# Kernel optimization log

Measured on AMD Instinct MI355X. Metric: run time of the kernel, lower is better.

## Reference

```python
import jax, jax.numpy as jnp
import numpy as np

B, T, F, D = 2, 1, 2112, 1024
H, DH = 8, 64
INNER = H * DH
NL = 721           # cls_dim(1) + num_latents(720)
VD = 64            # vis_dim // 4
DEPTH = 6
MAX_FRAMES = 2160
EPS = 1e-5
W_SCALE = 0.02


def _ln(x, g, b):
    m = jnp.mean(x, axis=-1, keepdims=True)
    v = jnp.mean(jnp.square(x - m), axis=-1, keepdims=True)
    return (x - m) * jax.lax.rsqrt(v + EPS) * g + b


def setup_inputs() -> dict:
    key = jax.random.key(0)
    ks = jax.random.split(key, 12)
    n = lambda k, shape, s=1.0: jax.random.normal(k, shape, dtype=jnp.float32) * s
    inp = {}
    inp['x'] = n(ks[0], (B, T, F, D))
    inp['split_sizes'] = jax.random.randint(ks[1], (B,), 0, F, dtype=jnp.int32)
    # resampler parameters (randn init like torch)
    inp['latents'] = n(ks[2], (NL, D))
    inp['spatial_embs'] = n(ks[3], (VD + 1, D))
    inp['frame_embs'] = n(ks[4], (MAX_FRAMES, D))
    # per-layer attention params (stacked over depth)
    inp['nm_g'] = jnp.ones((DEPTH, D)); inp['nm_b'] = jnp.zeros((DEPTH, D))
    inp['nl_g'] = jnp.ones((DEPTH, D)); inp['nl_b'] = jnp.zeros((DEPTH, D))
    inp['wq'] = n(ks[5], (DEPTH, D, INNER), W_SCALE)
    inp['wkv'] = n(ks[6], (DEPTH, D, 2 * INNER), W_SCALE)
    inp['wo'] = n(ks[7], (DEPTH, INNER, D), W_SCALE)
    # per-layer FFN params
    inp['ffn_g'] = jnp.ones((DEPTH, D)); inp['ffn_b'] = jnp.zeros((DEPTH, D))
    inp['ffw1'] = n(ks[8], (DEPTH, D, 4 * D), W_SCALE)
    inp['ffw2'] = n(ks[9], (DEPTH, 4 * D, D), W_SCALE)
    # final norm
    inp['final_g'] = jnp.ones((D,)); inp['final_b'] = jnp.zeros((D,))
    return inp


def reference(x, split_sizes, latents, spatial_embs, frame_embs,
              nm_g, nm_b, nl_g, nl_b, wq, wkv, wo,
              ffn_g, ffn_b, ffw1, ffw2, final_g, final_b):
    b, t, f, d = x.shape
    # spatial embeddings: first VD tokens get rows [:VD], rest get row [VD] broadcast
    add_sp = jnp.concatenate(
        [spatial_embs[:VD], jnp.broadcast_to(spatial_embs[VD:VD + 1], (f - VD, d))], axis=0)
    # frame embeddings: first VD tokens get row 0, frames get rows 1..f-VD
    add_fr = jnp.concatenate(
        [jnp.broadcast_to(frame_embs[0:1], (VD, d)), frame_embs[1:f - VD + 1]], axis=0)
    x = x + (add_sp + add_fr)  # broadcast over (b, t)

    lat = jnp.broadcast_to(latents, (b, t, NL, d))

    # variable-length mask over the x part of KV; latent positions never masked
    mask_x = jnp.arange(f)[None, :] >= split_sizes[:, None]              # (b, f)
    mask = jnp.concatenate([mask_x, jnp.zeros((b, NL), dtype=bool)], -1)  # (b, f+NL)
    mask = mask[:, None, None, None, :]                                   # (b,1,1,1,j)
    scale = DH ** -0.5

    for l in range(DEPTH):
        # --- PerceiverAttention ---
        xn = _ln(x, nm_g[l], nm_b[l])
        latn = _ln(lat, nl_g[l], nl_b[l])
        q = (latn @ wq[l]).reshape(b, t, NL, H, DH) * scale
        kv = jnp.concatenate([xn, latn], axis=-2) @ wkv[l]               # (b,t,f+NL,2*inner)
        k, v = jnp.split(kv, 2, axis=-1)
        k = k.reshape(b, t, f + NL, H, DH)
        v = v.reshape(b, t, f + NL, H, DH)
        sim = jnp.einsum('btihd,btjhd->bhtij', q, k)                     # (b,h,t,NL,f+NL)
        sim = sim - jax.lax.stop_gradient(jnp.max(sim, axis=-1, keepdims=True))
        sim = jnp.where(mask, -jnp.inf, sim)
        attn = jax.nn.softmax(sim, axis=-1)
        o = jnp.einsum('bhtij,btjhd->btihd', attn, v).reshape(b, t, NL, INNER)
        lat = lat + o @ wo[l]
        # --- FeedForward ---
        h1 = _ln(lat, ffn_g[l], ffn_b[l]) @ ffw1[l]
        lat = lat + jax.nn.gelu(h1, approximate=False) @ ffw2[l]

    return _ln(lat, final_g, final_b)
```

## Files before the change

kernel.cpp:

```cpp
#include <hip/hip_runtime.h>
#include <math.h>

constexpr int B = 2;
constexpr int F = 2112;
constexpr int D = 1024;
constexpr int H = 8;
constexpr int DH = 64;
constexpr int INNER = H * DH;
constexpr int NL = 721;
constexpr int NL_PAD = 768;
constexpr int MLAT = B * NL;
constexpr int MLAT_PAD = 1536;
constexpr int VD = 64;
constexpr int DEPTH = 6;
constexpr int FN = F + NL;
constexpr int FN_PAD = 2880;
constexpr int NBH = B * H;
constexpr int SKVMAX = 8;
constexpr int MX = B * F;
constexpr float EPS = 1e-5f;

typedef __bf16 bf16x8 __attribute__((ext_vector_type(8)));
typedef float  f32x4  __attribute__((ext_vector_type(4)));

static __device__ __forceinline__ unsigned short f2bf(float f)
{
    union { float f; unsigned int u; } x; x.f = f;
    unsigned int r = x.u + 0x7FFFu + ((x.u >> 16) & 1u);
    return (unsigned short)(r >> 16);
}
static __device__ __forceinline__ float bf2f(unsigned short u)
{
    union { unsigned int i; float f; } x; x.i = ((unsigned int)u) << 16; return x.f;
}

__device__ __forceinline__ void block_reduce_2(float& s, float& ss, float* red)
{
#pragma unroll
    for (int off = 32; off; off >>= 1) {
        s  += __shfl_xor(s, off);
        ss += __shfl_xor(ss, off);
    }
    int wv = threadIdx.x >> 6;
    if ((threadIdx.x & 63) == 0) { red[wv] = s; red[4 + wv] = ss; }
    __syncthreads();
    s  = red[0] + red[1] + red[2] + red[3];
    ss = red[4] + red[5] + red[6] + red[7];
}

__global__ __launch_bounds__(256) void emb_ln_kernel(
    const float* __restrict__ x, const float* __restrict__ sp_emb,
    const float* __restrict__ fr_emb, unsigned short* __restrict__ xhat)
{
    __shared__ float red[8];
    int r = blockIdx.x;
    int j = r % F;
    int t = threadIdx.x;
    const float4* xr = (const float4*)(x + (long)r * D);
    int spr = (j < VD) ? j : VD;
    int frr = (j < VD) ? 0 : (j - VD + 1);
    const float4* sp4 = (const float4*)(sp_emb + (long)spr * D);
    const float4* fr4 = (const float4*)(fr_emb + (long)frr * D);
    float4 v = xr[t], a = sp4[t], c = fr4[t];
    v.x += a.x + c.x; v.y += a.y + c.y; v.z += a.z + c.z; v.w += a.w + c.w;
    float s  = v.x + v.y + v.z + v.w;
    float ss = v.x*v.x + v.y*v.y + v.z*v.z + v.w*v.w;
    block_reduce_2(s, ss, red);
    float mean = s * (1.0f / D);
    float var  = ss * (1.0f / D) - mean * mean;
    float rstd = rsqrtf(var + EPS);
    ushort4 o;
    o.x = f2bf((v.x - mean) * rstd);
    o.y = f2bf((v.y - mean) * rstd);
    o.z = f2bf((v.z - mean) * rstd);
    o.w = f2bf((v.w - mean) * rstd);
    ((ushort4*)(xhat + (long)r * D))[t] = o;
}

__global__ __launch_bounds__(256) void prep_a_kernel(
    const unsigned short* __restrict__ xhat, const float* __restrict__ lat,
    const float* __restrict__ nmg, const float* __restrict__ nmb,
    const float* __restrict__ nlg, const float* __restrict__ nlb,
    unsigned short* __restrict__ xa, unsigned short* __restrict__ la)
{
    __shared__ float red[8];
    int r = blockIdx.x;
    int t = threadIdx.x;
    if (r < MX) {
        ushort4 u4 = ((const ushort4*)(xhat + (long)r * D))[t];
        float4 g4 = ((const float4*)nmg)[t];
        float4 b4 = ((const float4*)nmb)[t];
        ushort4 o;
        o.x = f2bf(bf2f(u4.x) * g4.x + b4.x);
        o.y = f2bf(bf2f(u4.y) * g4.y + b4.y);
        o.z = f2bf(bf2f(u4.z) * g4.z + b4.z);
        o.w = f2bf(bf2f(u4.w) * g4.w + b4.w);
        ((ushort4*)(xa + (long)r * D))[t] = o;
    } else {
        int rr = r - MX;
        float4 v = ((const float4*)(lat + (long)rr * D))[t];
        float s  = v.x + v.y + v.z + v.w;
        float ss = v.x*v.x + v.y*v.y + v.z*v.z + v.w*v.w;
        block_reduce_2(s, ss, red);
        float mean = s * (1.0f / D);
        float var  = ss * (1.0f / D) - mean * mean;
        float rstd = rsqrtf(var + EPS);
        float4 g4 = ((const float4*)nlg)[t];
        float4 b4 = ((const float4*)nlb)[t];
        ushort4 o;
        o.x = f2bf((v.x - mean) * rstd * g4.x + b4.x);
        o.y = f2bf((v.y - mean) * rstd * g4.y + b4.y);
        o.z = f2bf((v.z - mean) * rstd * g4.z + b4.z);
        o.w = f2bf((v.w - mean) * rstd * g4.w + b4.w);
        ((ushort4*)(la + (long)rr * D))[t] = o;
    }
}

__global__ __launch_bounds__(256) void rownorm_affine_bf16_kernel(
    const float* __restrict__ in, const float* __restrict__ g,
    const float* __restrict__ b, unsigned short* __restrict__ out)
{
    __shared__ float red[8];
    int r = blockIdx.x;
    int t = threadIdx.x;
    float4 v = ((const float4*)(in + (long)r * D))[t];
    float s  = v.x + v.y + v.z + v.w;
    float ss = v.x*v.x + v.y*v.y + v.z*v.z + v.w*v.w;
    block_reduce_2(s, ss, red);
    float mean = s * (1.0f / D);
    float var  = ss * (1.0f / D) - mean * mean;
    float rstd = rsqrtf(var + EPS);
    float4 g4 = ((const float4*)g)[t];
    float4 b4 = ((const float4*)b)[t];
    ushort4 o;
    o.x = f2bf((v.x - mean) * rstd * g4.x + b4.x);
    o.y = f2bf((v.y - mean) * rstd * g4.y + b4.y);
    o.z = f2bf((v.z - mean) * rstd * g4.z + b4.z);
    o.w = f2bf((v.w - mean) * rstd * g4.w + b4.w);
    ((ushort4*)(out + (long)r * D))[t] = o;
}

__global__ __launch_bounds__(256) void final_ln_kernel(
    const float* __restrict__ in, const float* __restrict__ g,
    const float* __restrict__ b, float* __restrict__ out)
{
    __shared__ float red[8];
    int r = blockIdx.x;
    int t = threadIdx.x;
    float4 v = ((const float4*)(in + (long)r * D))[t];
    float s  = v.x + v.y + v.z + v.w;
    float ss = v.x*v.x + v.y*v.y + v.z*v.z + v.w*v.w;
    block_reduce_2(s, ss, red);
    float mean = s * (1.0f / D);
    float var  = ss * (1.0f / D) - mean * mean;
    float rstd = rsqrtf(var + EPS);
    float4 g4 = ((const float4*)g)[t];
    float4 b4 = ((const float4*)b)[t];
    float4 o;
    o.x = (v.x - mean) * rstd * g4.x + b4.x;
    o.y = (v.y - mean) * rstd * g4.y + b4.y;
    o.z = (v.z - mean) * rstd * g4.z + b4.z;
    o.w = (v.w - mean) * rstd * g4.w + b4.w;
    ((float4*)(out + (long)r * D))[t] = o;
}

__global__ __launch_bounds__(256) void lat_init_kernel(
    const float* __restrict__ latents, float* __restrict__ lat)
{
    int r = blockIdx.x;
    int i = r % NL;
    int t = threadIdx.x;
    ((float4*)(lat + (long)r * D))[t] = ((const float4*)(latents + (long)i * D))[t];
}

constexpr long WL_LAT = 1536L * 1024;
constexpr long WL_WO  = 1024L * 512;
constexpr long WL_F1  = 4096L * 1024;
constexpr long WL_F2  = 1024L * 4096;
constexpr long WL_SZ  = WL_LAT + WL_WO + WL_F1 + WL_F2;

__device__ __forceinline__ void conv_tile64(
    const float* __restrict__ src, unsigned short* __restrict__ dst,
    int Kd, int Nd, int tn, int tk, float* lds)
{
    int t = threadIdx.x;
    int n0 = tn * 64, k0 = tk * 64;
#pragma unroll
    for (int p = 0; p < 16; ++p) {
        int idx = p * 256 + t;
        int kr = idx >> 6, nc = idx & 63;
        lds[nc * 65 + kr] = src[(long)(k0 + kr) * Nd + n0 + nc];
    }
    __syncthreads();
#pragma unroll
    for (int p = 0; p < 2; ++p) {
        int nl_ = p * 32 + (t >> 3);
        int kc  = t & 7;
        unsigned short u[8];
#pragma unroll
        for (int j = 0; j < 8; ++j)
            u[j] = f2bf(lds[nl_ * 65 + kc * 8 + j]);
        *(uint4*)(dst + (long)(n0 + nl_) * Kd + k0 + kc * 8) = *(uint4*)u;
    }
}

__global__ __launch_bounds__(256) void wt_conv_all_kernel(
    const float* __restrict__ wq, const float* __restrict__ wkv,
    const float* __restrict__ wo, const float* __restrict__ ffw1,
    const float* __restrict__ ffw2,
    unsigned short* __restrict__ wbuf, long wstride, int layer0)
{
    __shared__ float lds[64 * 65];
    int l = layer0 + blockIdx.y;
    unsigned short* wl = wbuf + (long)blockIdx.y * wstride;
    const float* wq_l   = wq   + (long)l * D * INNER;
    const float* wkv_l  = wkv  + (long)l * D * 2 * INNER;
    const float* wo_l   = wo   + (long)l * INNER * D;
    const float* ffw1_l = ffw1 + (long)l * D * 4 * D;
    const float* ffw2_l = ffw2 + (long)l * 4 * D * D;

    int T = blockIdx.x;
    if (T < 128) {
        conv_tile64(wq_l, wl, D, INNER, T & 7, T >> 3, lds);
    } else if (T < 384) {
        int Ti = T - 128;
        conv_tile64(wkv_l, wl + 512L * D, D, 2 * INNER, Ti & 15, Ti >> 4, lds);
    } else if (T < 512) {
        int Ti = T - 384;
        conv_tile64(wo_l, wl + WL_LAT, INNER, D, Ti & 15, Ti >> 4, lds);
    } else if (T < 1536) {
        int Ti = T - 512;
        conv_tile64(ffw1_l, wl + WL_LAT + WL_WO, D, 4 * D, Ti & 63, Ti >> 6, lds);
    } else {
        int Ti = T - 1536;
        conv_tile64(ffw2_l, wl + WL_LAT + WL_WO + WL_F1, 4 * D, D, Ti & 15, Ti >> 4, lds);
    }
}

__device__ __forceinline__ void load_set(
    const unsigned short* __restrict__ ap, const unsigned short* __restrict__ bp,
    long rs, int ko, bf16x8 (&av)[4], bf16x8 (&bv)[4])
{
#pragma unroll
    for (int q = 0; q < 4; ++q) {
        av[q] = *(const bf16x8*)(ap + q * rs + ko);
        bv[q] = *(const bf16x8*)(bp + q * rs + ko);
    }
}

__device__ __forceinline__ void mfma_set(
    const bf16x8 (&av)[4], const bf16x8 (&bv)[4], f32x4 (&acc)[4][4])
{
#pragma unroll
    for (int mm = 0; mm < 4; ++mm)
#pragma unroll
        for (int nn = 0; nn < 4; ++nn)
            acc[mm][nn] = __builtin_amdgcn_mfma_f32_16x16x32_bf16(av[mm], bv[nn], acc[mm][nn], 0, 0, 0);
}

__device__ __forceinline__ void gemm_core(
    const unsigned short* __restrict__ ap, const unsigned short* __restrict__ bp,
    long rs, int Kc, f32x4 (&acc)[4][4])
{
    bf16x8 aC[4], bC[4], aN[4], bN[4];
    load_set(ap, bp, rs, 0, aC, bC);
    for (int ko = 0; ko < Kc; ko += 64) {
        load_set(ap, bp, rs, ko + 32, aN, bN);
        mfma_set(aC, bC, acc);
        if (ko + 64 < Kc)
            load_set(ap, bp, rs, ko + 64, aC, bC);
        mfma_set(aN, bN, acc);
    }
}

__global__ __launch_bounds__(64) void qkv_fused_kernel(
    const unsigned short* __restrict__ la, const unsigned short* __restrict__ xa,
    const unsigned short* __restrict__ wlatT,
    unsigned short* __restrict__ qb, unsigned short* __restrict__ kb,
    unsigned short* __restrict__ vt)
{
    int lane = threadIdx.x;
    int lr = lane & 15, lg = lane >> 4;

    const unsigned short* A;
    const unsigned short* Bt;
    long m0, n0;
    int M, rpb, joff, qcols;
    int T = blockIdx.x;
    if (T < 552) {
        int bm = T % 23, bn = T / 23;
        A = la; Bt = wlatT;
        m0 = (long)bm * 64; n0 = (long)bn * 64;
        M = MLAT; rpb = NL; joff = F; qcols = 512;
    } else {
        int Ti = T - 552;
        int bm = Ti % 66, bn = Ti / 66;
        A = xa; Bt = wlatT + 512L * D;
        m0 = (long)bm * 64; n0 = (long)bn * 64;
        M = MX; rpb = F; joff = 0; qcols = 0;
    }

    const unsigned short* ap = A  + (m0 + lr) * D + lg * 8;
    const unsigned short* bp = Bt + (n0 + lr) * D + lg * 8;
    f32x4 acc[4][4] = {};
    gemm_core(ap, bp, 16L * D, D, acc);

#pragma unroll
    for (int mm = 0; mm < 4; ++mm) {
        long ar0 = m0 + mm * 16 + lg * 4;
        if (ar0 >= M) continue;
#pragma unroll
        for (int nn = 0; nn < 4; ++nn) {
            long col = n0 + nn * 16 + lr;
            f32x4 v = acc[mm][nn];
            if (col < qcols) {
#pragma unroll
                for (int r = 0; r < 4; ++r) {
                    long ar = ar0 + r;
                    if (ar < M) {
                        int bb = ar >= NL;
                        long i = ar - (bb ? NL : 0);
                        qb[((long)bb * NL_PAD + i) * INNER + col] = f2bf(v[r] * 0.125f);
                    }
                }
            } else {
                int c = (int)col - qcols;
                if (c < 512) {
#pragma unroll
                    for (int r = 0; r < 4; ++r) {
                        long ar = ar0 + r;
                        if (ar < M) {
                            int bb = ar >= rpb;
                            long i = ar - (bb ? rpb : 0);
                            kb[((long)bb * FN_PAD + joff + i) * INNER + c] = f2bf(v[r]);
                        }
                    }
                } else {
                    int d = c - 512;
                    int bb0 = ar0 >= rpb;
                    int bb3 = (ar0 + 3) >= rpb;
                    long i0 = ar0 - (bb0 ? rpb : 0);
                    long j0 = joff + i0;
                    if ((ar0 + 3 < M) && (bb0 == bb3) && ((j0 & 3) == 0)) {
                        ushort4 pk;
                        pk.x = f2bf(v[0]); pk.y = f2bf(v[1]);
                        pk.z = f2bf(v[2]); pk.w = f2bf(v[3]);
                        *(ushort4*)(vt + ((long)bb0 * INNER + d) * FN_PAD + j0) = pk;
                    } else {
#pragma unroll
                        for (int r = 0; r < 4; ++r) {
                            long ar = ar0 + r;
                            if (ar < M) {
                                int bb = ar >= rpb;
                                long i = ar - (bb ? rpb : 0);
                                vt[((long)bb * INNER + d) * FN_PAD + joff + i] = f2bf(v[r]);
                            }
                        }
                    }
                }
            }
        }
    }
}

#define MODE_RESA  0
#define MODE_GELU  1

__global__ __launch_bounds__(64) void gemm_split_kernel(
    const unsigned short* __restrict__ A, const unsigned short* __restrict__ Bt,
    void* __restrict__ C, int M, int K, int Kc, int mode, int ldc)
{
    int lane = threadIdx.x;
    int lr = lane & 15, lg = lane >> 4;
    long m0 = (long)blockIdx.x * 64;
    long n0 = (long)blockIdx.y * 64;
    int k0 = blockIdx.z * Kc;

    const unsigned short* ap = A  + (m0 + lr) * K + k0 + lg * 8;
    const unsigned short* bp = Bt + (n0 + lr) * K + k0 + lg * 8;
    f32x4 acc[4][4] = {};
    gemm_core(ap, bp, 16L * K, Kc, acc);

#pragma unroll
    for (int mm = 0; mm < 4; ++mm) {
        long ar0 = m0 + mm * 16 + lg * 4;
        if (ar0 >= M) continue;
#pragma unroll
        for (int nn = 0; nn < 4; ++nn) {
            long col = n0 + nn * 16 + lr;
            f32x4 v = acc[mm][nn];
            if (mode == MODE_RESA) {
                float* p = (float*)C;
#pragma unroll
                for (int r = 0; r < 4; ++r)
                    if (ar0 + r < M)
                        unsafeAtomicAdd(&p[(ar0 + r) * (long)ldc + col], v[r]);
            } else {
                unsigned short* p = (unsigned short*)C;
#pragma unroll
                for (int r = 0; r < 4; ++r)
                    if (ar0 + r < M) {
                        float val = v[r];
                        val = 0.5f * val * (1.0f + erff(val * 0.70710678118654752f));
                        p[(ar0 + r) * (long)ldc + col] = f2bf(val);
                    }
            }
        }
    }
}

__global__ __launch_bounds__(256) void attn_split_kernel(
    const unsigned short* __restrict__ qb, const unsigned short* __restrict__ kb,
    const unsigned short* __restrict__ vt, const int* __restrict__ split,
    float* __restrict__ po, float* __restrict__ pml, int skv)
{
    int bh = blockIdx.y;
    int b  = bh >> 3;
    int h  = bh & 7;
    int sidx = blockIdx.z;
    int w  = threadIdx.x >> 6;
    int lane = threadIdx.x & 63;
    int q0 = blockIdx.x * 64 + w * 16;
    if (q0 >= NL) return;

    __shared__ unsigned short p_lds[4][16 * 64];
    unsigned short* pl = p_lds[w];

    int lr = lane & 15;
    int lg = lane >> 4;

    bf16x8 qa0, qa1;
    {
        const unsigned short* qrow = qb + ((long)b * NL_PAD + q0 + lr) * INNER + h * 64;
        qa0 = *(const bf16x8*)(qrow + lg * 8);
        qa1 = *(const bf16x8*)(qrow + 32 + lg * 8);
    }

    f32x4 oacc[4] = {{0,0,0,0},{0,0,0,0},{0,0,0,0},{0,0,0,0}};
    float m[4]    = {-1e30f, -1e30f, -1e30f, -1e30f};
    float lsum[4] = {0.f, 0.f, 0.f, 0.f};

    int sp = split[b];
    if (sp < 0) sp = 0;
    if (sp > F) sp = F;
    int ntx = (sp + 63) >> 6;
    int ntot = ntx + 12;
    int t0 = (ntot * sidx) / skv;
    int t1 = (ntot * (sidx + 1)) / skv;

    for (int t = t0; t < t1; ++t) {
        int j0, limit;
        if (t < ntx) { j0 = t * 64;             limit = sp; }
        else         { j0 = F + (t - ntx) * 64; limit = FN; }

        f32x4 s[4] = {{0,0,0,0},{0,0,0,0},{0,0,0,0},{0,0,0,0}};
        const unsigned short* kbase =
            kb + ((long)b * FN_PAD + j0 + lr) * INNER + h * 64 + lg * 8;
#pragma unroll
        for (int st = 0; st < 4; ++st) {
            bf16x8 kf0 = *(const bf16x8*)(kbase + (long)st * 16 * INNER);
            bf16x8 kf1 = *(const bf16x8*)(kbase + (long)st * 16 * INNER + 32);
            s[st] = __builtin_amdgcn_mfma_f32_16x16x32_bf16(qa0, kf0, s[st], 0, 0, 0);
            s[st] = __builtin_amdgcn_mfma_f32_16x16x32_bf16(qa1, kf1, s[st], 0, 0, 0);
        }

        if (j0 + 64 > limit) {
#pragma unroll
            for (int st = 0; st < 4; ++st) {
                bool valid = (j0 + st * 16 + lr) < limit;
#pragma unroll
                for (int r = 0; r < 4; ++r)
                    s[st][r] = valid ? s[st][r] : -1e30f;
            }
        }

        float tm[4];
#pragma unroll
        for (int r = 0; r < 4; ++r)
            tm[r] = fmaxf(fmaxf(s[0][r], s[1][r]), fmaxf(s[2][r], s[3][r]));
#pragma unroll
        for (int off = 1; off < 16; off <<= 1) {
#pragma unroll
            for (int r = 0; r < 4; ++r)
                tm[r] = fmaxf(tm[r], __shfl_xor(tm[r], off));
        }
        float cr[4];
#pragma unroll
        for (int r = 0; r < 4; ++r) {
            float mn = fmaxf(m[r], tm[r]);
            cr[r] = __expf(m[r] - mn);
            m[r]  = mn;
        }
#pragma unroll
        for (int st = 0; st < 4; ++st)
#pragma unroll
            for (int r = 0; r < 4; ++r)
                s[st][r] = __expf(s[st][r] - m[r]);
        float ts[4];
#pragma unroll
        for (int r = 0; r < 4; ++r)
            ts[r] = (s[0][r] + s[1][r]) + (s[2][r] + s[3][r]);
#pragma unroll
        for (int off = 1; off < 16; off <<= 1) {
#pragma unroll
            for (int r = 0; r < 4; ++r)
                ts[r] += __shfl_xor(ts[r], off);
        }
#pragma unroll
        for (int r = 0; r < 4; ++r)
            lsum[r] = lsum[r] * cr[r] + ts[r];
#pragma unroll
        for (int nst = 0; nst < 4; ++nst)
#pragma unroll
            for (int r = 0; r < 4; ++r)
                oacc[nst][r] *= cr[r];

#pragma unroll
        for (int st = 0; st < 4; ++st)
#pragma unroll
            for (int r = 0; r < 4; ++r) {
                int row  = lg * 4 + r;
                int col  = st * 16 + lr;
                int byte = (row * 128 + col * 2) ^ ((row & 7) << 4);
                *(unsigned short*)((char*)pl + byte) = f2bf(s[st][r]);
            }

#pragma unroll
        for (int kk = 0; kk < 2; ++kk) {
            int row  = lr;
            int byte = (row * 128 + kk * 64 + lg * 16) ^ ((row & 7) << 4);
            bf16x8 pa = *(const bf16x8*)((char*)pl + byte);
#pragma unroll
            for (int nst = 0; nst < 4; ++nst) {
                const unsigned short* vp =
                    vt + ((long)bh * DH + nst * 16 + lr) * FN_PAD + j0 + kk * 32 + lg * 8;
                bf16x8 vf = *(const bf16x8*)vp;
                oacc[nst] = __builtin_amdgcn_mfma_f32_16x16x32_bf16(pa, vf, oacc[nst], 0, 0, 0);
            }
        }
    }

    long base = ((long)sidx * NBH + bh) * NL_PAD;
#pragma unroll
    for (int nst = 0; nst < 4; ++nst)
#pragma unroll
        for (int r = 0; r < 4; ++r) {
            int row = q0 + lg * 4 + r;
            if (row < NL)
                po[(base + row) * DH + nst * 16 + lr] = oacc[nst][r];
        }
    if (lr == 0) {
#pragma unroll
        for (int r = 0; r < 4; ++r) {
            int row = q0 + lg * 4 + r;
            if (row < NL) {
                pml[(base + row) * 2 + 0] = m[r];
                pml[(base + row) * 2 + 1] = lsum[r];
            }
        }
    }
}

__global__ __launch_bounds__(256) void attn_combine_kernel(
    const float* __restrict__ po, const float* __restrict__ pml,
    unsigned short* __restrict__ o, int skv)
{
    int row = blockIdx.x * 4 + (threadIdx.x >> 6);
    if (row >= NBH * NL) return;
    int lane = threadIdx.x & 63;
    int bh = row / NL;
    int i  = row - bh * NL;
    int b = bh >> 3, h = bh & 7;

    float m = -1e30f, l = 0.0f, acc = 0.0f;
    for (int s = 0; s < skv; ++s) {
        long base = ((long)s * NBH + bh) * NL_PAD + i;
        float ms = pml[base * 2 + 0];
        float ls = pml[base * 2 + 1];
        float os = po[base * DH + lane];
        float mn = fmaxf(m, ms);
        float c1 = __expf(m - mn);
        float c2 = __expf(ms - mn);
        acc = acc * c1 + os * c2;
        l   = l * c1 + ls * c2;
        m   = mn;
    }
    o[((long)b * NL + i) * INNER + h * 64 + lane] = f2bf(acc / l);
}

extern "C" void kernel_launch(void* const* d_in, const int* in_sizes, int n_in,
                              void* d_out, int out_size, void* d_ws, size_t ws_size,
                              hipStream_t stream)
{
    const float* x        = (const float*)d_in[0];
    const int*   split    = (const int*)d_in[1];
    const float* latents  = (const float*)d_in[2];
    const float* sp_emb   = (const float*)d_in[3];
    const float* fr_emb   = (const float*)d_in[4];
    const float* nm_g     = (const float*)d_in[5];
    const float* nm_b     = (const float*)d_in[6];
    const float* nl_g     = (const float*)d_in[7];
    const float* nl_b     = (const float*)d_in[8];
    const float* wq       = (const float*)d_in[9];
    const float* wkv      = (const float*)d_in[10];
    const float* wo       = (const float*)d_in[11];
    const float* ffw1     = (const float*)d_in[12 + 2];
    const float* ffn_g    = (const float*)d_in[12];
    const float* ffn_b    = (const float*)d_in[13];
    const float* ffw2     = (const float*)d_in[15];
    const float* final_g  = (const float*)d_in[16];
    const float* final_b  = (const float*)d_in[17];
    float* out = (float*)d_out;

    char* cur = (char*)d_ws;
    auto alloc = [&](size_t bytes) {
        void* p = (void*)cur;
        cur += (bytes + 255) & ~(size_t)255;
        return p;
    };

    unsigned short* xhat = (unsigned short*)alloc((long)MX * D * 2);
    float* lat  = (float*)alloc((long)B * NL * D * 4);
    unsigned short* la  = (unsigned short*)alloc((long)MLAT_PAD * D * 2);
    unsigned short* fa  = (unsigned short*)alloc((long)MLAT_PAD * D * 2);
    unsigned short* h1b = (unsigned short*)alloc((long)MLAT_PAD * 4 * D * 2);
    unsigned short* ob  = (unsigned short*)alloc((long)MLAT_PAD * INNER * 2);
    unsigned short* qb  = (unsigned short*)alloc((long)B * NL_PAD * INNER * 2);
    unsigned short* kb  = (unsigned short*)alloc((long)B * FN_PAD * INNER * 2);
    unsigned short* vt  = (unsigned short*)alloc((long)B * FN_PAD * INNER * 2);
    unsigned short* xa  = (unsigned short*)alloc((long)MX * D * 2);
    float* pml = (float*)alloc((long)SKVMAX * NBH * NL_PAD * 2 * 4);

    size_t fixed = (size_t)(cur - (char*)d_ws);
    const size_t po8 = ((size_t)8 * NBH * NL_PAD * DH * 4 + 255) & ~(size_t)255;
    const size_t po4 = ((size_t)4 * NBH * NL_PAD * DH * 4 + 255) & ~(size_t)255;
    const size_t wb6 = ((size_t)6 * WL_SZ * 2 + 255) & ~(size_t)255;
    const size_t wb1 = ((size_t)WL_SZ * 2 + 255) & ~(size_t)255;
    const size_t margin = 4096;

    int skv;
    bool hoist_w;
    if (fixed + po8 + wb6 + margin <= ws_size)      { skv = 8; hoist_w = true;  }
    else if (fixed + po4 + wb6 + margin <= ws_size) { skv = 4; hoist_w = true;  }
    else if (fixed + po8 + wb1 + margin <= ws_size) { skv = 8; hoist_w = false; }
    else                                            { skv = 4; hoist_w = false; }

    float* po = (float*)alloc(skv == 8 ? po8 : po4);
    unsigned short* wbuf = (unsigned short*)alloc(hoist_w ? wb6 : wb1);

    emb_ln_kernel<<<MX, 256, 0, stream>>>(x, sp_emb, fr_emb, xhat);
    lat_init_kernel<<<B * NL, 256, 0, stream>>>(latents, lat);

    if (hoist_w)
        wt_conv_all_kernel<<<dim3(2560, 6), 256, 0, stream>>>(
            wq, wkv, wo, ffw1, ffw2, wbuf, WL_SZ, 0);

    for (int l = 0; l < DEPTH; ++l) {
        unsigned short* wl = wbuf + (hoist_w ? (long)l * WL_SZ : 0);
        if (!hoist_w)
            wt_conv_all_kernel<<<dim3(2560, 1), 256, 0, stream>>>(
                wq, wkv, wo, ffw1, ffw2, wbuf, 0, l);

        unsigned short* wlatT = wl;
        unsigned short* woT   = wl + WL_LAT;
        unsigned short* f1T   = wl + WL_LAT + WL_WO;
        unsigned short* f2T   = wl + WL_LAT + WL_WO + WL_F1;

        prep_a_kernel<<<MX + MLAT, 256, 0, stream>>>(
            xhat, lat, nm_g + (long)l * D, nm_b + (long)l * D,
            nl_g + (long)l * D, nl_b + (long)l * D, xa, la);

        qkv_fused_kernel<<<1608, 64, 0, stream>>>(la, xa, wlatT, qb, kb, vt);

        attn_split_kernel<<<dim3(12, NBH, skv), 256, 0, stream>>>(
            qb, kb, vt, split, po, pml, skv);
        attn_combine_kernel<<<(NBH * NL + 3) / 4, 256, 0, stream>>>(po, pml, ob, skv);

        gemm_split_kernel<<<dim3(23, 16, 4), 64, 0, stream>>>(
            ob, woT, lat, MLAT, INNER, 128, MODE_RESA, D);

        rownorm_affine_bf16_kernel<<<MLAT, 256, 0, stream>>>(
            lat, ffn_g + (long)l * D, ffn_b + (long)l * D, fa);
        gemm_split_kernel<<<dim3(23, 64, 1), 64, 0, stream>>>(
            fa, f1T, h1b, MLAT, D, D, MODE_GELU, 4 * D);
        gemm_split_kernel<<<dim3(23, 16, 8), 64, 0, stream>>>(
            h1b, f2T, lat, MLAT, 4 * D, 512, MODE_RESA, D);
    }

    final_ln_kernel<<<MLAT, 256, 0, stream>>>(lat, final_g, final_b, out);
}
```

Before: 1.924 ms.

## Fuse per-layer kernel sequence into persistent mega-kernel with grid barriers

Replaces the eight-plus kernel launches per layer with a single persistent kernel of 512 blocks. Each stage is processed as a wave-level work loop and the stages are separated by an atomic-counter grid barrier. Row layernorms become per-wave shuffle reductions. Attention split-KV is fixed at 4 and weights are always hoisted for all layers. This is meant to remove launch overhead and tail effects, but it risks deadlock if not all 512 blocks are co-resident, and it loses per-stage grid tuning.

```diff
diff --git a/kernel.cpp b/kernel.cpp
--- a/kernel.cpp
+++ b/kernel.cpp
@@ -16,8 +16,9 @@
 constexpr int FN = F + NL;
 constexpr int FN_PAD = 2880;
 constexpr int NBH = B * H;
-constexpr int SKVMAX = 8;
+constexpr int SKV = 4;
 constexpr int MX = B * F;
+constexpr int MEGA_G = 512;
 constexpr float EPS = 1e-5f;
 
 typedef __bf16 bf16x8 __attribute__((ext_vector_type(8)));
@@ -77,69 +78,6 @@
     ((ushort4*)(xhat + (long)r * D))[t] = o;
 }
 
-__global__ __launch_bounds__(256) void prep_a_kernel(
-    const unsigned short* __restrict__ xhat, const float* __restrict__ lat,
-    const float* __restrict__ nmg, const float* __restrict__ nmb,
-    const float* __restrict__ nlg, const float* __restrict__ nlb,
-    unsigned short* __restrict__ xa, unsigned short* __restrict__ la)
-{
-    __shared__ float red[8];
-    int r = blockIdx.x;
-    int t = threadIdx.x;
-    if (r < MX) {
-        ushort4 u4 = ((const ushort4*)(xhat + (long)r * D))[t];
-        float4 g4 = ((const float4*)nmg)[t];
-        float4 b4 = ((const float4*)nmb)[t];
-        ushort4 o;
-        o.x = f2bf(bf2f(u4.x) * g4.x + b4.x);
-        o.y = f2bf(bf2f(u4.y) * g4.y + b4.y);
-        o.z = f2bf(bf2f(u4.z) * g4.z + b4.z);
-        o.w = f2bf(bf2f(u4.w) * g4.w + b4.w);
-        ((ushort4*)(xa + (long)r * D))[t] = o;
-    } else {
-        int rr = r - MX;
-        float4 v = ((const float4*)(lat + (long)rr * D))[t];
-        float s  = v.x + v.y + v.z + v.w;
-        float ss = v.x*v.x + v.y*v.y + v.z*v.z + v.w*v.w;
-        block_reduce_2(s, ss, red);
-        float mean = s * (1.0f / D);
-        float var  = ss * (1.0f / D) - mean * mean;
-        float rstd = rsqrtf(var + EPS);
-        float4 g4 = ((const float4*)nlg)[t];
-        float4 b4 = ((const float4*)nlb)[t];
-        ushort4 o;
-        o.x = f2bf((v.x - mean) * rstd * g4.x + b4.x);
-        o.y = f2bf((v.y - mean) * rstd * g4.y + b4.y);
-        o.z = f2bf((v.z - mean) * rstd * g4.z + b4.z);
-        o.w = f2bf((v.w - mean) * rstd * g4.w + b4.w);
-        ((ushort4*)(la + (long)rr * D))[t] = o;
-    }
-}
-
-__global__ __launch_bounds__(256) void rownorm_affine_bf16_kernel(
-    const float* __restrict__ in, const float* __restrict__ g,
-    const float* __restrict__ b, unsigned short* __restrict__ out)
-{
-    __shared__ float red[8];
-    int r = blockIdx.x;
-    int t = threadIdx.x;
-    float4 v = ((const float4*)(in + (long)r * D))[t];
-    float s  = v.x + v.y + v.z + v.w;
-    float ss = v.x*v.x + v.y*v.y + v.z*v.z + v.w*v.w;
-    block_reduce_2(s, ss, red);
-    float mean = s * (1.0f / D);
-    float var  = ss * (1.0f / D) - mean * mean;
-    float rstd = rsqrtf(var + EPS);
-    float4 g4 = ((const float4*)g)[t];
-    float4 b4 = ((const float4*)b)[t];
-    ushort4 o;
-    o.x = f2bf((v.x - mean) * rstd * g4.x + b4.x);
-    o.y = f2bf((v.y - mean) * rstd * g4.y + b4.y);
-    o.z = f2bf((v.z - mean) * rstd * g4.z + b4.z);
-    o.w = f2bf((v.w - mean) * rstd * g4.w + b4.w);
-    ((ushort4*)(out + (long)r * D))[t] = o;
-}
-
 __global__ __launch_bounds__(256) void final_ln_kernel(
     const float* __restrict__ in, const float* __restrict__ g,
     const float* __restrict__ b, float* __restrict__ out)
@@ -165,8 +103,10 @@
 }
 
 __global__ __launch_bounds__(256) void lat_init_kernel(
-    const float* __restrict__ latents, float* __restrict__ lat)
-{
+    const float* __restrict__ latents, float* __restrict__ lat,
+    unsigned* __restrict__ cnt)
+{
+    if (blockIdx.x == 0 && threadIdx.x == 0) *cnt = 0u;
     int r = blockIdx.x;
     int i = r % NL;
     int t = threadIdx.x;
@@ -207,12 +147,11 @@
 __global__ __launch_bounds__(256) void wt_conv_all_kernel(
     const float* __restrict__ wq, const float* __restrict__ wkv,
     const float* __restrict__ wo, const float* __restrict__ ffw1,
-    const float* __restrict__ ffw2,
-    unsigned short* __restrict__ wbuf, long wstride, int layer0)
+    const float* __restrict__ ffw2, unsigned short* __restrict__ wbuf)
 {
     __shared__ float lds[64 * 65];
-    int l = layer0 + blockIdx.y;
-    unsigned short* wl = wbuf + (long)blockIdx.y * wstride;
+    int l = blockIdx.y;
+    unsigned short* wl = wbuf + (long)l * WL_SZ;
     const float* wq_l   = wq   + (long)l * D * INNER;
     const float* wkv_l  = wkv  + (long)l * D * 2 * INNER;
     const float* wo_l   = wo   + (long)l * INNER * D;
@@ -237,6 +176,74 @@
     }
 }
 
+__device__ __forceinline__ void grid_bar(unsigned* cnt, unsigned& epoch, int G)
+{
+    __syncthreads();
+    if (threadIdx.x == 0) {
+        __threadfence();
+        atomicAdd(cnt, 1u);
+        epoch += (unsigned)G;
+        int guard = 0;
+        while (__hip_atomic_load(cnt, __ATOMIC_RELAXED, __HIP_MEMORY_SCOPE_AGENT) < epoch) {
+            __builtin_amdgcn_s_sleep(2);
+            if (++guard > (1 << 26)) break;
+        }
+        __threadfence();
+    }
+    __syncthreads();
+}
+
+__device__ __forceinline__ void wave_ln_aff(
+    const float* __restrict__ in, const float* __restrict__ g,
+    const float* __restrict__ b, unsigned short* __restrict__ out, int lane)
+{
+    float4 v[4];
+    float s = 0.f, ss = 0.f;
+#pragma unroll
+    for (int p = 0; p < 4; ++p) {
+        v[p] = ((const float4*)in)[lane + p * 64];
+        s  += v[p].x + v[p].y + v[p].z + v[p].w;
+        ss += v[p].x*v[p].x + v[p].y*v[p].y + v[p].z*v[p].z + v[p].w*v[p].w;
+    }
+#pragma unroll
+    for (int off = 32; off; off >>= 1) {
+        s  += __shfl_xor(s, off);
+        ss += __shfl_xor(ss, off);
+    }
+    float mean = s * (1.0f / D);
+    float var  = ss * (1.0f / D) - mean * mean;
+    float rstd = rsqrtf(var + EPS);
+#pragma unroll
+    for (int p = 0; p < 4; ++p) {
+        float4 g4 = ((const float4*)g)[lane + p * 64];
+        float4 b4 = ((const float4*)b)[lane + p * 64];
+        ushort4 o;
+        o.x = f2bf((v[p].x - mean) * rstd * g4.x + b4.x);
+        o.y = f2bf((v[p].y - mean) * rstd * g4.y + b4.y);
+        o.z = f2bf((v[p].z - mean) * rstd * g4.z + b4.z);
+        o.w = f2bf((v[p].w - mean) * rstd * g4.w + b4.w);
+        ((ushort4*)out)[lane + p * 64] = o;
+    }
+}
+
+__device__ __forceinline__ void wave_aff(
+    const unsigned short* __restrict__ in, const float* __restrict__ g,
+    const float* __restrict__ b, unsigned short* __restrict__ out, int lane)
+{
+#pragma unroll
+    for (int p = 0; p < 4; ++p) {
+        ushort4 u4 = ((const ushort4*)in)[lane + p * 64];
+        float4 g4 = ((const float4*)g)[lane + p * 64];
+        float4 b4 = ((const float4*)b)[lane + p * 64];
+        ushort4 o;
+        o.x = f2bf(bf2f(u4.x) * g4.x + b4.x);
+        o.y = f2bf(bf2f(u4.y) * g4.y + b4.y);
+        o.z = f2bf(bf2f(u4.z) * g4.z + b4.z);
+        o.w = f2bf(bf2f(u4.w) * g4.w + b4.w);
+        ((ushort4*)out)[lane + p * 64] = o;
+    }
+}
+
 __device__ __forceinline__ void load_set(
     const unsigned short* __restrict__ ap, const unsigned short* __restrict__ bp,
     long rs, int ko, bf16x8 (&av)[4], bf16x8 (&bv)[4])
@@ -273,20 +280,17 @@
     }
 }
 
-__global__ __launch_bounds__(64) void qkv_fused_kernel(
+__device__ void qkv_tile(int T,
     const unsigned short* __restrict__ la, const unsigned short* __restrict__ xa,
     const unsigned short* __restrict__ wlatT,
     unsigned short* __restrict__ qb, unsigned short* __restrict__ kb,
-    unsigned short* __restrict__ vt)
-{
-    int lane = threadIdx.x;
+    unsigned short* __restrict__ vt, int lane)
+{
     int lr = lane & 15, lg = lane >> 4;
-
     const unsigned short* A;
     const unsigned short* Bt;
     long m0, n0;
     int M, rpb, joff, qcols;
-    int T = blockIdx.x;
     if (T < 552) {
         int bm = T % 23, bn = T / 23;
         A = la; Bt = wlatT;
@@ -363,24 +367,18 @@
     }
 }
 
-#define MODE_RESA  0
-#define MODE_GELU  1
-
-__global__ __launch_bounds__(64) void gemm_split_kernel(
+__device__ void gemm_tile_resa(
     const unsigned short* __restrict__ A, const unsigned short* __restrict__ Bt,
-    void* __restrict__ C, int M, int K, int Kc, int mode, int ldc)
-{
-    int lane = threadIdx.x;
+    float* __restrict__ C, int M, int K, int Kc, int ldc,
+    int bm, int bn, int kz, int lane)
+{
     int lr = lane & 15, lg = lane >> 4;
-    long m0 = (long)blockIdx.x * 64;
-    long n0 = (long)blockIdx.y * 64;
-    int k0 = blockIdx.z * Kc;
-
+    long m0 = (long)bm * 64, n0 = (long)bn * 64;
+    int k0 = kz * Kc;
     const unsigned short* ap = A  + (m0 + lr) * K + k0 + lg * 8;
     const unsigned short* bp = Bt + (n0 + lr) * K + k0 + lg * 8;
     f32x4 acc[4][4] = {};
     gemm_core(ap, bp, 16L * K, Kc, acc);
-
 #pragma unroll
     for (int mm = 0; mm < 4; ++mm) {
         long ar0 = m0 + mm * 16 + lg * 4;
@@ -389,42 +387,56 @@
         for (int nn = 0; nn < 4; ++nn) {
             long col = n0 + nn * 16 + lr;
             f32x4 v = acc[mm][nn];
-            if (mode == MODE_RESA) {
-                float* p = (float*)C;
-#pragma unroll
-                for (int r = 0; r < 4; ++r)
-                    if (ar0 + r < M)
-                        unsafeAtomicAdd(&p[(ar0 + r) * (long)ldc + col], v[r]);
-            } else {
-                unsigned short* p = (unsigned short*)C;
-#pragma unroll
-                for (int r = 0; r < 4; ++r)
-                    if (ar0 + r < M) {
-                        float val = v[r];
-                        val = 0.5f * val * (1.0f + erff(val * 0.70710678118654752f));
-                        p[(ar0 + r) * (long)ldc + col] = f2bf(val);
-                    }
-            }
-        }
-    }
-}
-
-__global__ __launch_bounds__(256) void attn_split_kernel(
+#pragma unroll
+            for (int r = 0; r < 4; ++r)
+                if (ar0 + r < M)
+                    unsafeAtomicAdd(&C[(ar0 + r) * (long)ldc + col], v[r]);
+        }
+    }
+}
+
+__device__ void gemm_tile_gelu(
+    const unsigned short* __restrict__ A, const unsigned short* __restrict__ Bt,
+    unsigned short* __restrict__ C, int M, int K, int ldc,
+    int bm, int bn, int lane)
+{
+    int lr = lane & 15, lg = lane >> 4;
+    long m0 = (long)bm * 64, n0 = (long)bn * 64;
+    const unsigned short* ap = A  + (m0 + lr) * K + lg * 8;
+    const unsigned short* bp = Bt + (n0 + lr) * K + lg * 8;
+    f32x4 acc[4][4] = {};
+    gemm_core(ap, bp, 16L * K, K, acc);
+#pragma unroll
+    for (int mm = 0; mm < 4; ++mm) {
+        long ar0 = m0 + mm * 16 + lg * 4;
+        if (ar0 >= M) continue;
+#pragma unroll
+        for (int nn = 0; nn < 4; ++nn) {
+            long col = n0 + nn * 16 + lr;
+            f32x4 v = acc[mm][nn];
+#pragma unroll
+            for (int r = 0; r < 4; ++r)
+                if (ar0 + r < M) {
+                    float val = v[r];
+                    val = 0.5f * val * (1.0f + erff(val * 0.70710678118654752f));
+                    C[(ar0 + r) * (long)ldc + col] = f2bf(val);
+                }
+        }
+    }
+}
+
+__device__ void attn_unit(int u,
     const unsigned short* __restrict__ qb, const unsigned short* __restrict__ kb,
     const unsigned short* __restrict__ vt, const int* __restrict__ split,
-    float* __restrict__ po, float* __restrict__ pml, int skv)
-{
-    int bh = blockIdx.y;
-    int b  = bh >> 3;
-    int h  = bh & 7;
-    int sidx = blockIdx.z;
-    int w  = threadIdx.x >> 6;
-    int lane = threadIdx.x & 63;
-    int q0 = blockIdx.x * 64 + w * 16;
+    float* __restrict__ po, float* __restrict__ pml,
+    unsigned short* pl, int lane)
+{
+    int q16  = u % 48;
+    int bh   = (u / 48) % NBH;
+    int sidx = u / (48 * NBH);
+    int q0 = q16 * 16;
     if (q0 >= NL) return;
-
-    __shared__ unsigned short p_lds[4][16 * 64];
-    unsigned short* pl = p_lds[w];
+    int b = bh >> 3, h = bh & 7;
 
     int lr = lane & 15;
     int lg = lane >> 4;
@@ -445,8 +457,8 @@
     if (sp > F) sp = F;
     int ntx = (sp + 63) >> 6;
     int ntot = ntx + 12;
-    int t0 = (ntot * sidx) / skv;
-    int t1 = (ntot * (sidx + 1)) / skv;
+    int t0 = (ntot * sidx) / SKV;
+    int t1 = (ntot * (sidx + 1)) / SKV;
 
     for (int t = t0; t < t1; ++t) {
         int j0, limit;
@@ -561,19 +573,17 @@
     }
 }
 
-__global__ __launch_bounds__(256) void attn_combine_kernel(
+__device__ void combine_unit(int u,
     const float* __restrict__ po, const float* __restrict__ pml,
-    unsigned short* __restrict__ o, int skv)
-{
-    int row = blockIdx.x * 4 + (threadIdx.x >> 6);
-    if (row >= NBH * NL) return;
-    int lane = threadIdx.x & 63;
-    int bh = row / NL;
-    int i  = row - bh * NL;
+    unsigned short* __restrict__ o, int lane)
+{
+    int bh = u / NL;
+    int i  = u - bh * NL;
     int b = bh >> 3, h = bh & 7;
 
     float m = -1e30f, l = 0.0f, acc = 0.0f;
-    for (int s = 0; s < skv; ++s) {
+#pragma unroll
+    for (int s = 0; s < SKV; ++s) {
         long base = ((long)s * NBH + bh) * NL_PAD + i;
         float ms = pml[base * 2 + 0];
         float ls = pml[base * 2 + 1];
@@ -586,6 +596,82 @@
         m   = mn;
     }
     o[((long)b * NL + i) * INNER + h * 64 + lane] = f2bf(acc / l);
+}
+
+__global__ __launch_bounds__(256, 2) void mega_kernel(
+    const unsigned short* __restrict__ xhat, float* __restrict__ lat,
+    const float* __restrict__ nm_g, const float* __restrict__ nm_b,
+    const float* __restrict__ nl_g, const float* __restrict__ nl_b,
+    const float* __restrict__ ffn_g, const float* __restrict__ ffn_b,
+    const unsigned short* __restrict__ wbuf,
+    unsigned short* __restrict__ xa, unsigned short* __restrict__ la,
+    unsigned short* __restrict__ fa, unsigned short* __restrict__ h1b,
+    unsigned short* __restrict__ ob, unsigned short* __restrict__ qb,
+    unsigned short* __restrict__ kb, unsigned short* __restrict__ vt,
+    float* __restrict__ po, float* __restrict__ pml,
+    const int* __restrict__ split, unsigned* __restrict__ cnt)
+{
+    __shared__ unsigned short p_lds[4][16 * 64];
+    const int G = MEGA_G;
+    int w = threadIdx.x >> 6, lane = threadIdx.x & 63;
+    int gw = blockIdx.x * 4 + w;
+    int GW = G * 4;
+    unsigned epoch = 0;
+
+    for (int l = 0; l < DEPTH; ++l) {
+        const unsigned short* wl    = wbuf + (long)l * WL_SZ;
+        const unsigned short* wlatT = wl;
+        const unsigned short* woT   = wl + WL_LAT;
+        const unsigned short* f1T   = wl + WL_LAT + WL_WO;
+        const unsigned short* f2T   = wl + WL_LAT + WL_WO + WL_F1;
+
+        for (int u = gw; u < MX + MLAT; u += GW) {
+            if (u < MX)
+                wave_aff(xhat + (long)u * D, nm_g + (long)l * D, nm_b + (long)l * D,
+                         xa + (long)u * D, lane);
+            else {
+                int r = u - MX;
+                wave_ln_aff(lat + (long)r * D, nl_g + (long)l * D, nl_b + (long)l * D,
+                            la + (long)r * D, lane);
+            }
+        }
+        grid_bar(cnt, epoch, G);
+
+        for (int u = gw; u < 1608; u += GW)
+            qkv_tile(u, la, xa, wlatT, qb, kb, vt, lane);
+        grid_bar(cnt, epoch, G);
+
+        for (int u = gw; u < 48 * NBH * SKV; u += GW)
+            attn_unit(u, qb, kb, vt, split, po, pml, p_lds[w], lane);
+        grid_bar(cnt, epoch, G);
+
+        for (int u = gw; u < NBH * NL; u += GW)
+            combine_unit(u, po, pml, ob, lane);
+        grid_bar(cnt, epoch, G);
+
+        for (int u = gw; u < 23 * 16 * 4; u += GW) {
+            int bm = u % 23, bn = (u / 23) & 15, kz = u / 368;
+            gemm_tile_resa(ob, woT, lat, MLAT, INNER, 128, D, bm, bn, kz, lane);
+        }
+        grid_bar(cnt, epoch, G);
+
+        for (int u = gw; u < MLAT; u += GW)
+            wave_ln_aff(lat + (long)u * D, ffn_g + (long)l * D, ffn_b + (long)l * D,
+                        fa + (long)u * D, lane);
+        grid_bar(cnt, epoch, G);
+
+        for (int u = gw; u < 23 * 64; u += GW) {
+            int bm = u % 23, bn = u / 23;
+            gemm_tile_gelu(fa, f1T, h1b, MLAT, D, 4 * D, bm, bn, lane);
+        }
+        grid_bar(cnt, epoch, G);
+
+        for (int u = gw; u < 23 * 16 * 8; u += GW) {
+            int bm = u % 23, bn = (u / 23) & 15, kz = u / 368;
+            gemm_tile_resa(h1b, f2T, lat, MLAT, 4 * D, 512, D, bm, bn, kz, lane);
+        }
+        grid_bar(cnt, epoch, G);
+    }
 }
 
 extern "C" void kernel_launch(void* const* d_in, const int* in_sizes, int n_in,
@@ -604,9 +690,9 @@
     const float* wq       = (const float*)d_in[9];
     const float* wkv      = (const float*)d_in[10];
     const float* wo       = (const float*)d_in[11];
-    const float* ffw1     = (const float*)d_in[12 + 2];
     const float* ffn_g    = (const float*)d_in[12];
     const float* ffn_b    = (const float*)d_in[13];
+    const float* ffw1     = (const float*)d_in[14];
     const float* ffw2     = (const float*)d_in[15];
     const float* final_g  = (const float*)d_in[16];
     const float* final_b  = (const float*)d_in[17];
@@ -629,63 +715,18 @@
     unsigned short* kb  = (unsigned short*)alloc((long)B * FN_PAD * INNER * 2);
     unsigned short* vt  = (unsigned short*)alloc((long)B * FN_PAD * INNER * 2);
     unsigned short* xa  = (unsigned short*)alloc((long)MX * D * 2);
-    float* pml = (float*)alloc((long)SKVMAX * NBH * NL_PAD * 2 * 4);
-
-    size_t fixed = (size_t)(cur - (char*)d_ws);
-    const size_t po8 = ((size_t)8 * NBH * NL_PAD * DH * 4 + 255) & ~(size_t)255;
-    const size_t po4 = ((size_t)4 * NBH * NL_PAD * DH * 4 + 255) & ~(size_t)255;
-    const size_t wb6 = ((size_t)6 * WL_SZ * 2 + 255) & ~(size_t)255;
-    const size_t wb1 = ((size_t)WL_SZ * 2 + 255) & ~(size_t)255;
-    const size_t margin = 4096;
-
-    int skv;
-    bool hoist_w;
-    if (fixed + po8 + wb6 + margin <= ws_size)      { skv = 8; hoist_w = true;  }
-    else if (fixed + po4 + wb6 + margin <= ws_size) { skv = 4; hoist_w = true;  }
-    else if (fixed + po8 + wb1 + margin <= ws_size) { skv = 8; hoist_w = false; }
-    else                                            { skv = 4; hoist_w = false; }
-
-    float* po = (float*)alloc(skv == 8 ? po8 : po4);
-    unsigned short* wbuf = (unsigned short*)alloc(hoist_w ? wb6 : wb1);
+    float* po  = (float*)alloc((long)SKV * NBH * NL_PAD * DH * 4);
+    float* pml = (float*)alloc((long)SKV * NBH * NL_PAD * 2 * 4);
+    unsigned* cnt = (unsigned*)alloc(256);
+    unsigned short* wbuf = (unsigned short*)alloc((size_t)6 * WL_SZ * 2);
 
     emb_ln_kernel<<<MX, 256, 0, stream>>>(x, sp_emb, fr_emb, xhat);
-    lat_init_kernel<<<B * NL, 256, 0, stream>>>(latents, lat);
-
-    if (hoist_w)
-        wt_conv_all_kernel<<<dim3(2560, 6), 256, 0, stream>>>(
-            wq, wkv, wo, ffw1, ffw2, wbuf, WL_SZ, 0);
-
-    for (int l = 0; l < DEPTH; ++l) {
-        unsigned short* wl = wbuf + (hoist_w ? (long)l * WL_SZ : 0);
-        if (!hoist_w)
-            wt_conv_all_kernel<<<dim3(2560, 1), 256, 0, stream>>>(
-                wq, wkv, wo, ffw1, ffw2, wbuf, 0, l);
-
-        unsigned short* wlatT = wl;
-        unsigned short* woT   = wl + WL_LAT;
-        unsigned short* f1T   = wl + WL_LAT + WL_WO;
-        unsigned short* f2T   = wl + WL_LAT + WL_WO + WL_F1;
-
-        prep_a_kernel<<<MX + MLAT, 256, 0, stream>>>(
-            xhat, lat, nm_g + (long)l * D, nm_b + (long)l * D,
-            nl_g + (long)l * D, nl_b + (long)l * D, xa, la);
-
-        qkv_fused_kernel<<<1608, 64, 0, stream>>>(la, xa, wlatT, qb, kb, vt);
-
-        attn_split_kernel<<<dim3(12, NBH, skv), 256, 0, stream>>>(
-            qb, kb, vt, split, po, pml, skv);
-        attn_combine_kernel<<<(NBH * NL + 3) / 4, 256, 0, stream>>>(po, pml, ob, skv);
-
-        gemm_split_kernel<<<dim3(23, 16, 4), 64, 0, stream>>>(
-            ob, woT, lat, MLAT, INNER, 128, MODE_RESA, D);
-
-        rownorm_affine_bf16_kernel<<<MLAT, 256, 0, stream>>>(
-            lat, ffn_g + (long)l * D, ffn_b + (long)l * D, fa);
-        gemm_split_kernel<<<dim3(23, 64, 1), 64, 0, stream>>>(
-            fa, f1T, h1b, MLAT, D, D, MODE_GELU, 4 * D);
-        gemm_split_kernel<<<dim3(23, 16, 8), 64, 0, stream>>>(
-            h1b, f2T, lat, MLAT, 4 * D, 512, MODE_RESA, D);
-    }
+    lat_init_kernel<<<B * NL, 256, 0, stream>>>(latents, lat, cnt);
+    wt_conv_all_kernel<<<dim3(2560, 6), 256, 0, stream>>>(wq, wkv, wo, ffw1, ffw2, wbuf);
+
+    mega_kernel<<<MEGA_G, 256, 0, stream>>>(
+        xhat, lat, nm_g, nm_b, nl_g, nl_b, ffn_g, ffn_b, wbuf,
+        xa, la, fa, h1b, ob, qb, kb, vt, po, pml, split, cnt);
 
     final_ln_kernel<<<MLAT, 256, 0, stream>>>(lat, final_g, final_b, out);
 }
```

New measurement: 4.590 ms. 2.39x slower.
